# Kernel optimization log

Measured on AMD Instinct MI355X. Metric: run time of the kernel, lower is better.

## Reference

```python
import jax, jax.numpy as jnp
import numpy as np

DIM = 8      # channels (from CxWxW_Attention(8, 4, False))
HEADS = 4    # num_heads
EPS = 1e-12  # torch F.normalize eps


def setup_inputs() -> dict:
    key = jax.random.key(0)
    k0, k1, k2, k3 = jax.random.split(key, 4)
    b, c, h, w = 16, DIM, 512, 512
    x = jax.random.normal(k0, (b, c, h, w), jnp.float32)
    # 1x1 conv producing qkv (bias=False): weight (3c, c)
    w_qkv = jax.random.normal(k1, (3 * c, c), jnp.float32) * 0.1
    # 3x3 depthwise conv on qkv, groups=3c: weight (3c, 1, 3, 3)
    w_dw = jax.random.normal(k2, (3 * c, 1, 3, 3), jnp.float32) * 0.1
    # 1x1 projection out: weight (c, c)
    w_out = jax.random.normal(k3, (c, c), jnp.float32) * 0.1
    # per-head learned temperature, init ones; broadcasts over (b, head, c, w, w)
    temperature = jnp.ones((HEADS, 1, 1, 1), jnp.float32)
    return dict(x=x, w_qkv=w_qkv, w_dw=w_dw, w_out=w_out, temperature=temperature)


def _dwconv3x3(x, wgt):
    # depthwise 3x3, padding=1, groups = channels
    C = x.shape[1]
    return jax.lax.conv_general_dilated(
        x, wgt, window_strides=(1, 1), padding=((1, 1), (1, 1)),
        dimension_numbers=("NCHW", "OIHW", "NCHW"), feature_group_count=C)


def _l2norm(t):
    # torch.nn.functional.normalize along last dim
    n = jnp.sqrt(jnp.sum(t * t, axis=-1, keepdims=True))
    return t / jnp.maximum(n, EPS)


def reference(x, w_qkv, w_dw, w_out, temperature):
    b, c, h, w = x.shape
    heads, ch = HEADS, c // HEADS
    # qkv = dwconv3x3(conv1x1(x))
    qkv = jnp.einsum("bchw,oc->bohw", x, w_qkv)
    qkv = _dwconv3x3(qkv, w_dw)
    q, k, v = jnp.split(qkv, 3, axis=1)
    # rearrange 'b (head ch) h w -> b head ch w h' : width attends, height = feature
    def split_heads(t):
        return t.reshape(b, heads, ch, h, w).transpose(0, 1, 2, 4, 3)
    q, k, v = split_heads(q), split_heads(k), split_heads(v)
    q = _l2norm(q)
    k = _l2norm(k)
    # attention map of shape (b, head, ch, W, W)  -> the 'C x W x W' attention
    attn = jnp.einsum("bncwh,bncvh->bncwv", q, k) * temperature
    attn = jax.nn.softmax(attn, axis=-1)
    out = jnp.einsum("bncwv,bncvh->bncwh", attn, v)  # (b, head, ch, w, h)
    # rearrange back 'b head ch w h -> b (head ch) h w'
    out = out.transpose(0, 1, 2, 4, 3).reshape(b, c, h, w)
    return jnp.einsum("bchw,oc->bohw", out, w_out)
```

## Files before the change

kernel.cpp:

```cpp
#include <hip/hip_runtime.h>
#include <hip/hip_bf16.h>

typedef __attribute__((ext_vector_type(4))) float f32x4;
typedef __attribute__((ext_vector_type(2))) float f32x2;
typedef __attribute__((ext_vector_type(8))) short s16x8;
typedef __attribute__((ext_vector_type(4))) short s16x4;
typedef __attribute__((ext_vector_type(4))) unsigned short u16x4;

#define HW 512
#define NSLICE 128

__global__ __launch_bounds__(256) void qkv_fused(
    const float* __restrict__ x, const float* __restrict__ wqkv,
    const float* __restrict__ wdw,
    __hip_bfloat16* __restrict__ qT, __hip_bfloat16* __restrict__ kT,
    __hip_bfloat16* __restrict__ vS,
    float* __restrict__ qss, float* __restrict__ kss)
{
  const int b = blockIdx.y;
  const int tile = blockIdx.x;
  const int h0 = (tile >> 4) * 32;
  const int w0 = (tile & 15) * 32;
  const int tid = threadIdx.x;

  __shared__ float ts[4][1156][2];
  __shared__ __hip_bfloat16 ot[8][32][36];
  __shared__ float colsq[4][8][32];
  __shared__ float wq_s[24][8];
  __shared__ float wd_s[24][12];

  if (tid < 192) wq_s[tid >> 3][tid & 7] = wqkv[tid];
  if (tid < 216) wd_s[tid / 9][tid % 9] = wdw[tid];

  float xr[5][8];
  #pragma unroll
  for (int p = 0; p < 5; ++p) {
    int i = tid + p * 256;
    if (i < 1156) {
      int ih = h0 - 1 + i / 34, iw = w0 - 1 + i % 34;
      bool ok = (ih >= 0 && ih < HW && iw >= 0 && iw < HW);
      #pragma unroll
      for (int c = 0; c < 8; ++c) {
        xr[p][c] = ok ? x[((size_t)(b * 8 + c) * HW + ih) * HW + iw] : 0.f;
      }
    }
  }
  __syncthreads();

  const int tw = tid & 31;
  const int th = tid >> 5;
  const int lane = tid & 63;
  const int wv = tid >> 6;

  #pragma unroll
  for (int g = 0; g < 3; ++g) {
    #pragma unroll
    for (int p = 0; p < 5; ++p) {
      int i = tid + p * 256;
      if (i < 1156) {
        #pragma unroll
        for (int op = 0; op < 4; ++op) {
          const int o = g * 8 + op * 2;
          float a0 = 0.f, a1 = 0.f;
          #pragma unroll
          for (int c = 0; c < 8; ++c) {
            a0 += xr[p][c] * wq_s[o][c];
            a1 += xr[p][c] * wq_s[o + 1][c];
          }
          ts[op][i][0] = a0;
          ts[op][i][1] = a1;
        }
      }
    }
    __syncthreads();

    #pragma unroll
    for (int op = 0; op < 4; ++op) {
      const int o = g * 8 + op * 2;
      float w2[6][3][2];
      #pragma unroll
      for (int r = 0; r < 6; ++r)
        #pragma unroll
        for (int c = 0; c < 3; ++c) {
          f32x2 v = *(const f32x2*)&ts[op][(4 * th + r) * 34 + tw + c][0];
          w2[r][c][0] = v[0];
          w2[r][c][1] = v[1];
        }
      float o0[4], o1[4];
      #pragma unroll
      for (int r = 0; r < 4; ++r) { o0[r] = 0.f; o1[r] = 0.f; }
      #pragma unroll
      for (int di = 0; di < 3; ++di)
        #pragma unroll
        for (int dj = 0; dj < 3; ++dj) {
          const float wd0 = wd_s[o][di * 3 + dj];
          const float wd1 = wd_s[o + 1][di * 3 + dj];
          #pragma unroll
          for (int r = 0; r < 4; ++r) {
            o0[r] += w2[r + di][dj][0] * wd0;
            o1[r] += w2[r + di][dj][1] * wd1;
          }
        }
      if (g < 2) {
        float s0 = o0[0] * o0[0] + o0[1] * o0[1] + o0[2] * o0[2] + o0[3] * o0[3];
        float s1 = o1[0] * o1[0] + o1[1] * o1[1] + o1[2] * o1[2] + o1[3] * o1[3];
        s0 += __shfl_xor(s0, 32);
        s1 += __shfl_xor(s1, 32);
        if (lane < 32) {
          colsq[wv][op * 2][tw] = s0;
          colsq[wv][op * 2 + 1][tw] = s1;
        }
        #pragma unroll
        for (int r = 0; r < 4; ++r) {
          ot[op * 2][tw][4 * th + r] = __float2bfloat16(o0[r]);
          ot[op * 2 + 1][tw][4 * th + r] = __float2bfloat16(o1[r]);
        }
      } else {
        #pragma unroll
        for (int r = 0; r < 4; ++r) {
          ot[op * 2][4 * th + r][tw] = __float2bfloat16(o0[r]);
          ot[op * 2 + 1][4 * th + r][tw] = __float2bfloat16(o1[r]);
        }
      }
    }
    __syncthreads();

    {
      const int rr = tid >> 3, cc = tid & 7;
      #pragma unroll
      for (int o = 0; o < 8; ++o) {
        s16x4 v = *(const s16x4*)&ot[o][rr][cc * 4];
        const size_t sb = (size_t)(b * 8 + o) * HW * HW;
        if (g == 0) {
          *(s16x4*)(qT + sb + (size_t)(h0 >> 5) * HW * 32 + (size_t)(w0 + rr) * 32 + cc * 4) = v;
        } else if (g == 1) {
          *(s16x4*)(kT + sb + (size_t)(h0 >> 5) * HW * 32 + (size_t)(w0 + rr) * 32 + cc * 4) = v;
        } else {
          *(s16x4*)(vS + sb + (size_t)(w0 >> 5) * HW * 32 + (size_t)(h0 + rr) * 32 + cc * 4) = v;
        }
      }
    }
    if (g < 2) {
      const int o = tid >> 5, w = tid & 31;
      float s = colsq[0][o][w] + colsq[1][o][w] + colsq[2][o][w] + colsq[3][o][w];
      float* dst = (g == 0 ? qss : kss) + (size_t)(b * 8 + o) * HW + w0 + w;
      atomicAdd(dst, s);
    }
  }
}

#define QROW 1040
#define LDS_QP   0
#define OFF_RMAX 66560
#define OFF_RSUM 68608
#define OFF_RMAXF 70656
#define OFF_RSINV 70912
#define OFF_SQ   71168
#define OFF_SK   71424
#define ATTN_LDS_SIZE 73472

#define GL4(D, VOFF, BASE) \
  asm volatile("global_load_dwordx4 %0, %1, %2 offset:0"    : "=v"(D[0]) : "v"(VOFF), "s"(BASE)); \
  asm volatile("global_load_dwordx4 %0, %1, %2 offset:1024" : "=v"(D[1]) : "v"(VOFF), "s"(BASE)); \
  asm volatile("global_load_dwordx4 %0, %1, %2 offset:2048" : "=v"(D[2]) : "v"(VOFF), "s"(BASE)); \
  asm volatile("global_load_dwordx4 %0, %1, %2 offset:3072" : "=v"(D[3]) : "v"(VOFF), "s"(BASE));

#define LOADSETK(BF, CHN) { \
  const char* bk_ = ks + (size_t)(CHN) * 32768; \
  GL4(BF, voffK, bk_) }

#define LOADSETV(VF, CHN) { \
  const char* bv_ = vs + (size_t)(CHN) * 32768; \
  GL4(VF, voffK, bv_) }

#define WAITV(N) \
  asm volatile("s_waitcnt vmcnt(" #N ")"); \
  __builtin_amdgcn_sched_barrier(0);

#define LDSQ(QF, S) { \
    const int cq_ = (S) * 64 + klo; \
    _Pragma("unroll") for (int m_ = 0; m_ < 4; ++m_) \
      QF[m_] = *(const s16x8*)(ldsQ + (m_ * 16 + arow) * QROW + cq_); }

#define LOADP(AF, S) { \
    const int cbp_ = (S) * 64 + klo; \
    _Pragma("unroll") for (int m_ = 0; m_ < 4; ++m_) { \
      const int row_ = m_ * 16 + arow; \
      AF[m_] = *(const s16x8*)(ldsP + row_ * 1024 + (cbp_ ^ ((row_ & 7) << 4))); } }
#define MFMA16(AF, BF, ACC) { \
    _Pragma("unroll") for (int m_ = 0; m_ < 4; ++m_) \
      _Pragma("unroll") for (int n_ = 0; n_ < 4; ++n_) \
        ACC[m_][n_] = __builtin_amdgcn_mfma_f32_16x16x32_bf16(AF[m_], BF[n_], ACC[m_][n_], 0, 0, 0); }

__global__ __launch_bounds__(512, 1) void attn_kernel(
    const __hip_bfloat16* __restrict__ qT, const __hip_bfloat16* __restrict__ kT,
    const __hip_bfloat16* __restrict__ vS, __hip_bfloat16* __restrict__ Obuf,
    const float* __restrict__ qss, const float* __restrict__ kss,
    const float* __restrict__ temp)
{
  extern __shared__ char smem[];
  char* ldsQ = smem + LDS_QP;
  char* ldsP = smem + LDS_QP;
  float* red_max  = (float*)(smem + OFF_RMAX);
  float* red_sum  = (float*)(smem + OFF_RSUM);
  float* red_maxf = (float*)(smem + OFF_RMAXF);
  float* rsinv    = (float*)(smem + OFF_RSINV);
  float* sq_l     = (float*)(smem + OFF_SQ);
  float* sk_l     = (float*)(smem + OFF_SK);

  const int tid = threadIdx.x;
  const int lane = tid & 63;
  const int wv = tid >> 6;
  const int p = blockIdx.x;
  const int slice = (p & 7) + 8 * (p >> 6);
  const int rblk = (p >> 3) & 7;
  const int w0 = rblk * 64;
  const size_t sbase = (size_t)slice * HW * HW;
  const char* qs = (const char*)(qT + sbase);
  const char* ks = (const char*)(kT + sbase);
  const char* vs = (const char*)(vS + sbase);

  const int klo = (lane >> 4) << 4;
  const int arow = lane & 15;
  const int voffK = (wv * 64 + arow) * 64 + klo;

  {
    const int r = tid >> 3;
    const int seg = tid & 7;
    #pragma unroll
    for (int i = 0; i < 8; ++i) {
      const int chn_i = seg * 2 + (i >> 2);
      s16x8 v = *(const s16x8*)(qs + (size_t)chn_i * 32768 + (size_t)(w0 + r) * 64 + (i & 3) * 16);
      *(s16x8*)(ldsQ + r * QROW + seg * 128 + i * 16) = v;
    }
  }
  const float tmp = temp[(slice & 7) >> 1];
  if (tid < 64) sq_l[tid] = tmp / fmaxf(sqrtf(qss[(size_t)slice * HW + w0 + tid]), 1e-12f);
  sk_l[tid] = 1.f / fmaxf(sqrtf(kss[(size_t)slice * HW + tid]), 1e-12f);
  __syncthreads();

  f32x4 acc[4][4];
  #pragma unroll
  for (int m = 0; m < 4; ++m)
    #pragma unroll
    for (int n = 0; n < 4; ++n) acc[m][n] = (f32x4){0.f, 0.f, 0.f, 0.f};
  __builtin_amdgcn_sched_barrier(0);

  s16x8 bfA[4], bfB[4], bfC[4], bfD[4];
  LOADSETK(bfA, 0)
  LOADSETK(bfB, 1)
  LOADSETK(bfC, 2)
  LOADSETK(bfD, 3)

  #pragma unroll
  for (int g = 0; g < 3; ++g) {
    { s16x8 qf[4]; LDSQ(qf, 4 * g + 0) WAITV(12) MFMA16(qf, bfA, acc) } LOADSETK(bfA, 4 * g + 4)
    { s16x8 qf[4]; LDSQ(qf, 4 * g + 1) WAITV(12) MFMA16(qf, bfB, acc) } LOADSETK(bfB, 4 * g + 5)
    { s16x8 qf[4]; LDSQ(qf, 4 * g + 2) WAITV(12) MFMA16(qf, bfC, acc) } LOADSETK(bfC, 4 * g + 6)
    { s16x8 qf[4]; LDSQ(qf, 4 * g + 3) WAITV(12) MFMA16(qf, bfD, acc) } LOADSETK(bfD, 4 * g + 7)
  }
  { s16x8 qf[4]; LDSQ(qf, 12) WAITV(12) MFMA16(qf, bfA, acc) }
  { s16x8 qf[4]; LDSQ(qf, 13) WAITV(8)  MFMA16(qf, bfB, acc) }
  { s16x8 qf[4]; LDSQ(qf, 14) WAITV(4)  MFMA16(qf, bfC, acc) }
  { s16x8 qf[4]; LDSQ(qf, 15) WAITV(0)  MFMA16(qf, bfD, acc) }
  __syncthreads();

  float srow[4][4], scol[4];
  #pragma unroll
  for (int m = 0; m < 4; ++m)
    #pragma unroll
    for (int r = 0; r < 4; ++r)
      srow[m][r] = sq_l[m * 16 + ((lane >> 4) << 2) + r];
  #pragma unroll
  for (int n = 0; n < 4; ++n) scol[n] = sk_l[wv * 64 + n * 16 + (lane & 15)];

  float rmax[4][4];
  #pragma unroll
  for (int m = 0; m < 4; ++m)
    #pragma unroll
    for (int r = 0; r < 4; ++r) {
      float mx = -1e30f;
      #pragma unroll
      for (int n = 0; n < 4; ++n) {
        float v = acc[m][n][r] * srow[m][r] * scol[n];
        acc[m][n][r] = v;
        mx = fmaxf(mx, v);
      }
      mx = fmaxf(mx, __shfl_xor(mx, 1));
      mx = fmaxf(mx, __shfl_xor(mx, 2));
      mx = fmaxf(mx, __shfl_xor(mx, 4));
      mx = fmaxf(mx, __shfl_xor(mx, 8));
      rmax[m][r] = mx;
    }
  if ((lane & 15) == 0) {
    #pragma unroll
    for (int m = 0; m < 4; ++m)
      #pragma unroll
      for (int r = 0; r < 4; ++r)
        red_max[(m * 16 + ((lane >> 4) << 2) + r) * 8 + wv] = rmax[m][r];
  }
  __syncthreads();
  if (tid < 64) {
    float mx = red_max[tid * 8];
    #pragma unroll
    for (int g = 1; g < 8; ++g) mx = fmaxf(mx, red_max[tid * 8 + g]);
    red_maxf[tid] = mx;
  }
  __syncthreads();

  float gmax[4][4];
  #pragma unroll
  for (int m = 0; m < 4; ++m)
    #pragma unroll
    for (int r = 0; r < 4; ++r)
      gmax[m][r] = red_maxf[m * 16 + ((lane >> 4) << 2) + r];

  s16x8 vfA[4], vfB[4], vfC[4], vfD[4];
  LOADSETV(vfA, 0)
  LOADSETV(vfB, 1)
  LOADSETV(vfC, 2)
  LOADSETV(vfD, 3)

  float rs[4][4];
  #pragma unroll
  for (int m = 0; m < 4; ++m)
    #pragma unroll
    for (int r = 0; r < 4; ++r) rs[m][r] = 0.f;
  #pragma unroll
  for (int m = 0; m < 4; ++m)
    #pragma unroll
    for (int n = 0; n < 4; ++n)
      #pragma unroll
      for (int r = 0; r < 4; ++r) {
        int row = m * 16 + ((lane >> 4) << 2) + r;
        int col = wv * 64 + n * 16 + (lane & 15);
        float pv = __expf(acc[m][n][r] - gmax[m][r]);
        rs[m][r] += pv;
        *(__hip_bfloat16*)(ldsP + row * 1024 + ((col * 2) ^ ((row & 7) << 4))) =
            __float2bfloat16(pv);
      }
  #pragma unroll
  for (int m = 0; m < 4; ++m)
    #pragma unroll
    for (int r = 0; r < 4; ++r) {
      float s = rs[m][r];
      s += __shfl_xor(s, 1);
      s += __shfl_xor(s, 2);
      s += __shfl_xor(s, 4);
      s += __shfl_xor(s, 8);
      if ((lane & 15) == 0)
        red_sum[(m * 16 + ((lane >> 4) << 2) + r) * 8 + wv] = s;
    }
  __syncthreads();
  if (tid < 64) {
    float s = 0.f;
    #pragma unroll
    for (int g = 0; g < 8; ++g) s += red_sum[tid * 8 + g];
    rsinv[tid] = 1.f / s;
  }

  f32x4 acc2[4][4];
  #pragma unroll
  for (int m = 0; m < 4; ++m)
    #pragma unroll
    for (int n = 0; n < 4; ++n) acc2[m][n] = (f32x4){0.f, 0.f, 0.f, 0.f};

  #pragma unroll
  for (int g = 0; g < 3; ++g) {
    { s16x8 pf[4]; LOADP(pf, 4 * g + 0) WAITV(12) MFMA16(pf, vfA, acc2) } LOADSETV(vfA, 4 * g + 4)
    { s16x8 pf[4]; LOADP(pf, 4 * g + 1) WAITV(12) MFMA16(pf, vfB, acc2) } LOADSETV(vfB, 4 * g + 5)
    { s16x8 pf[4]; LOADP(pf, 4 * g + 2) WAITV(12) MFMA16(pf, vfC, acc2) } LOADSETV(vfC, 4 * g + 6)
    { s16x8 pf[4]; LOADP(pf, 4 * g + 3) WAITV(12) MFMA16(pf, vfD, acc2) } LOADSETV(vfD, 4 * g + 7)
  }
  { s16x8 pf[4]; LOADP(pf, 12) WAITV(12) MFMA16(pf, vfA, acc2) }
  { s16x8 pf[4]; LOADP(pf, 13) WAITV(8)  MFMA16(pf, vfB, acc2) }
  { s16x8 pf[4]; LOADP(pf, 14) WAITV(4)  MFMA16(pf, vfC, acc2) }
  { s16x8 pf[4]; LOADP(pf, 15) WAITV(0)  MFMA16(pf, vfD, acc2) }
  __syncthreads();

  float rinv[4][4];
  #pragma unroll
  for (int m = 0; m < 4; ++m)
    #pragma unroll
    for (int r = 0; r < 4; ++r)
      rinv[m][r] = rsinv[m * 16 + ((lane >> 4) << 2) + r];

  char* ldsO = ldsP + wv * 8192;
  #pragma unroll
  for (int m = 0; m < 4; ++m)
    #pragma unroll
    for (int n = 0; n < 4; ++n)
      #pragma unroll
      for (int r = 0; r < 4; ++r) {
        int row = m * 16 + ((lane >> 4) << 2) + r;
        int col = n * 16 + (lane & 15);
        *(__hip_bfloat16*)(ldsO + row * 128 + col * 2) =
            __float2bfloat16(acc2[m][n][r] * rinv[m][r]);
      }
  __syncthreads();
  __hip_bfloat16* ob = Obuf + sbase + (size_t)w0 * HW + wv * 64;
  #pragma unroll
  for (int it = 0; it < 8; ++it) {
    int row = it * 8 + (lane >> 3);
    int c = (lane & 7) << 4;
    s16x8 v = *(const s16x8*)(ldsO + row * 128 + c);
    *(s16x8*)((char*)ob + (size_t)row * 1024 + c) = v;
  }
}

__global__ __launch_bounds__(256) void proj_kernel(
    const __hip_bfloat16* __restrict__ Obuf, const float* __restrict__ wout,
    float* __restrict__ out)
{
  const int b = blockIdx.y;
  const int t = blockIdx.x;
  const int h0 = (t >> 5) * 64;
  const int w0 = (t & 31) * 16;
  const int tid = threadIdx.x;
  __shared__ float os[8][16][65];
  __shared__ float wo_s[64];
  if (tid < 64) wo_s[tid] = wout[tid];
  {
    int r = tid >> 4;
    int c4 = (tid & 15) * 4;
    #pragma unroll
    for (int o = 0; o < 8; ++o) {
      const __hip_bfloat16* p = Obuf + ((size_t)(b * 8 + o) * HW + w0 + r) * HW + h0 + c4;
      u16x4 v = *(const u16x4*)p;
      #pragma unroll
      for (int i = 0; i < 4; ++i)
        os[o][r][c4 + i] = __uint_as_float((unsigned)v[i] << 16);
    }
  }
  __syncthreads();
  const int w = tid & 15;
  #pragma unroll
  for (int ih = 0; ih < 4; ++ih) {
    int h = ih * 16 + (tid >> 4);
    float ov[8];
    #pragma unroll
    for (int o = 0; o < 8; ++o) ov[o] = os[o][w][h];
    #pragma unroll
    for (int jo = 0; jo < 8; ++jo) {
      float a = 0.f;
      #pragma unroll
      for (int o = 0; o < 8; ++o) a += ov[o] * wo_s[jo * 8 + o];
      out[((size_t)(b * 8 + jo) * HW + h0 + h) * HW + w0 + w] = a;
    }
  }
}

extern "C" void kernel_launch(void* const* d_in, const int* in_sizes, int n_in,
                              void* d_out, int out_size, void* d_ws, size_t ws_size,
                              hipStream_t stream) {
  (void)in_sizes; (void)n_in; (void)out_size; (void)ws_size;
  const float* x    = (const float*)d_in[0];
  const float* wqkv = (const float*)d_in[1];
  const float* wdw  = (const float*)d_in[2];
  const float* wout = (const float*)d_in[3];
  const float* temp = (const float*)d_in[4];
  float* out = (float*)d_out;

  char* ws = (char*)d_ws;
  const size_t plane = (size_t)NSLICE * HW * HW * 2;
  __hip_bfloat16* qT = (__hip_bfloat16*)(ws);
  __hip_bfloat16* kT = (__hip_bfloat16*)(ws + plane);
  __hip_bfloat16* vS = (__hip_bfloat16*)(ws + 2 * plane);
  __hip_bfloat16* Ob = (__hip_bfloat16*)(ws + 3 * plane);
  float* qss = (float*)(ws + 4 * plane);
  float* kss = (float*)(ws + 4 * plane + (size_t)NSLICE * HW * 4);

  hipMemsetAsync(qss, 0, 2 * (size_t)NSLICE * HW * 4, stream);
  qkv_fused<<<dim3(256, 16), 256, 0, stream>>>(x, wqkv, wdw, qT, kT, vS, qss, kss);
  hipFuncSetAttribute((const void*)attn_kernel,
                      hipFuncAttributeMaxDynamicSharedMemorySize, ATTN_LDS_SIZE);
  attn_kernel<<<dim3(1024), 512, ATTN_LDS_SIZE, stream>>>(qT, kT, vS, Ob, qss, kss, temp);
  proj_kernel<<<dim3(256, 16), 256, 0, stream>>>(Ob, wout, out);
}
```

Measured before the change: 323.0 us.

## Compute 1x1 conv per thread in registers, drop LDS staging and transpose tiles

The qkv kernel now stages raw x into shared memory once, and each thread loads its own 6x3x8 input window into registers. It recomputes the 1x1 projection for its halo locally instead of writing projected channels to shared memory and syncing per group. Outputs go straight to global memory without the shared-memory transpose buffer, and the per-column squared-norm atomics are batched once at the end. This removes most barriers and LDS traffic, at the cost of redundant 1x1 conv arithmetic on halo pixels, higher register pressure, and narrower, less coalesced global stores for V.

```diff
diff --git a/kernel.cpp b/kernel.cpp
--- a/kernel.cpp
+++ b/kernel.cpp
@@ -10,7 +10,9 @@
 #define HW 512
 #define NSLICE 128
 
-__global__ __launch_bounds__(256) void qkv_fused(
+union B4 { s16x4 v; __hip_bfloat16 e[4]; };
+
+__global__ __launch_bounds__(256, 2) void qkv_fused(
     const float* __restrict__ x, const float* __restrict__ wqkv,
     const float* __restrict__ wdw,
     __hip_bfloat16* __restrict__ qT, __hip_bfloat16* __restrict__ kT,
@@ -23,16 +25,14 @@
   const int w0 = (tile & 15) * 32;
   const int tid = threadIdx.x;
 
-  __shared__ float ts[4][1156][2];
-  __shared__ __hip_bfloat16 ot[8][32][36];
-  __shared__ float colsq[4][8][32];
+  __shared__ float xs[8][1156];
+  __shared__ float colsq[4][16][32];
   __shared__ float wq_s[24][8];
-  __shared__ float wd_s[24][12];
+  __shared__ float wd_s[24][9];
 
   if (tid < 192) wq_s[tid >> 3][tid & 7] = wqkv[tid];
   if (tid < 216) wd_s[tid / 9][tid % 9] = wdw[tid];
 
-  float xr[5][8];
   #pragma unroll
   for (int p = 0; p < 5; ++p) {
     int i = tid + p * 256;
@@ -40,9 +40,8 @@
       int ih = h0 - 1 + i / 34, iw = w0 - 1 + i % 34;
       bool ok = (ih >= 0 && ih < HW && iw >= 0 && iw < HW);
       #pragma unroll
-      for (int c = 0; c < 8; ++c) {
-        xr[p][c] = ok ? x[((size_t)(b * 8 + c) * HW + ih) * HW + iw] : 0.f;
-      }
+      for (int c = 0; c < 8; ++c)
+        xs[c][i] = ok ? x[((size_t)(b * 8 + c) * HW + ih) * HW + iw] : 0.f;
     }
   }
   __syncthreads();
@@ -52,39 +51,32 @@
   const int lane = tid & 63;
   const int wv = tid >> 6;
 
-  #pragma unroll
+  float xr[8][6][3];
+  #pragma unroll
+  for (int c = 0; c < 8; ++c)
+    #pragma unroll
+    for (int wr = 0; wr < 6; ++wr)
+      #pragma unroll
+      for (int wc = 0; wc < 3; ++wc)
+        xr[c][wr][wc] = xs[c][(4 * th + wr) * 34 + tw + wc];
+
   for (int g = 0; g < 3; ++g) {
     #pragma unroll
-    for (int p = 0; p < 5; ++p) {
-      int i = tid + p * 256;
-      if (i < 1156) {
+    for (int op = 0; op < 4; ++op) {
+      const int o = g * 8 + op * 2;
+      float t0[6][3], t1[6][3];
+      #pragma unroll
+      for (int wr = 0; wr < 6; ++wr)
         #pragma unroll
-        for (int op = 0; op < 4; ++op) {
-          const int o = g * 8 + op * 2;
+        for (int wc = 0; wc < 3; ++wc) {
           float a0 = 0.f, a1 = 0.f;
           #pragma unroll
           for (int c = 0; c < 8; ++c) {
-            a0 += xr[p][c] * wq_s[o][c];
-            a1 += xr[p][c] * wq_s[o + 1][c];
+            a0 += xr[c][wr][wc] * wq_s[o][c];
+            a1 += xr[c][wr][wc] * wq_s[o + 1][c];
           }
-          ts[op][i][0] = a0;
-          ts[op][i][1] = a1;
-        }
-      }
-    }
-    __syncthreads();
-
-    #pragma unroll
-    for (int op = 0; op < 4; ++op) {
-      const int o = g * 8 + op * 2;
-      float w2[6][3][2];
-      #pragma unroll
-      for (int r = 0; r < 6; ++r)
-        #pragma unroll
-        for (int c = 0; c < 3; ++c) {
-          f32x2 v = *(const f32x2*)&ts[op][(4 * th + r) * 34 + tw + c][0];
-          w2[r][c][0] = v[0];
-          w2[r][c][1] = v[1];
+          t0[wr][wc] = a0;
+          t1[wr][wc] = a1;
         }
       float o0[4], o1[4];
       #pragma unroll
@@ -97,55 +89,50 @@
           const float wd1 = wd_s[o + 1][di * 3 + dj];
           #pragma unroll
           for (int r = 0; r < 4; ++r) {
-            o0[r] += w2[r + di][dj][0] * wd0;
-            o1[r] += w2[r + di][dj][1] * wd1;
+            o0[r] += t0[r + di][dj] * wd0;
+            o1[r] += t1[r + di][dj] * wd1;
           }
         }
       if (g < 2) {
-        float s0 = o0[0] * o0[0] + o0[1] * o0[1] + o0[2] * o0[2] + o0[3] * o0[3];
-        float s1 = o1[0] * o1[0] + o1[1] * o1[1] + o1[2] * o1[2] + o1[3] * o1[3];
+        float s0 = o0[0]*o0[0] + o0[1]*o0[1] + o0[2]*o0[2] + o0[3]*o0[3];
+        float s1 = o1[0]*o1[0] + o1[1]*o1[1] + o1[2]*o1[2] + o1[3]*o1[3];
         s0 += __shfl_xor(s0, 32);
         s1 += __shfl_xor(s1, 32);
         if (lane < 32) {
-          colsq[wv][op * 2][tw] = s0;
-          colsq[wv][op * 2 + 1][tw] = s1;
+          colsq[wv][g * 8 + op * 2][tw] = s0;
+          colsq[wv][g * 8 + op * 2 + 1][tw] = s1;
         }
+        B4 u0, u1;
         #pragma unroll
         for (int r = 0; r < 4; ++r) {
-          ot[op * 2][tw][4 * th + r] = __float2bfloat16(o0[r]);
-          ot[op * 2 + 1][tw][4 * th + r] = __float2bfloat16(o1[r]);
+          u0.e[r] = __float2bfloat16(o0[r]);
+          u1.e[r] = __float2bfloat16(o1[r]);
         }
+        __hip_bfloat16* base = (g == 0) ? qT : kT;
+        size_t a0i = (size_t)(b * 8 + op * 2) * HW * HW
+                   + (size_t)(h0 >> 5) * HW * 32 + (size_t)(w0 + tw) * 32 + 4 * th;
+        *(s16x4*)(base + a0i) = u0.v;
+        *(s16x4*)(base + a0i + (size_t)HW * HW) = u1.v;
       } else {
+        __hip_bfloat16* vb0 = vS + (size_t)(b * 8 + op * 2) * HW * HW
+                            + (size_t)(w0 >> 5) * HW * 32 + (size_t)(h0 + 4 * th) * 32 + tw;
+        __hip_bfloat16* vb1 = vb0 + (size_t)HW * HW;
         #pragma unroll
         for (int r = 0; r < 4; ++r) {
-          ot[op * 2][4 * th + r][tw] = __float2bfloat16(o0[r]);
-          ot[op * 2 + 1][4 * th + r][tw] = __float2bfloat16(o1[r]);
+          vb0[r * 32] = __float2bfloat16(o0[r]);
+          vb1[r * 32] = __float2bfloat16(o1[r]);
         }
       }
     }
-    __syncthreads();
-
-    {
-      const int rr = tid >> 3, cc = tid & 7;
-      #pragma unroll
-      for (int o = 0; o < 8; ++o) {
-        s16x4 v = *(const s16x4*)&ot[o][rr][cc * 4];
-        const size_t sb = (size_t)(b * 8 + o) * HW * HW;
-        if (g == 0) {
-          *(s16x4*)(qT + sb + (size_t)(h0 >> 5) * HW * 32 + (size_t)(w0 + rr) * 32 + cc * 4) = v;
-        } else if (g == 1) {
-          *(s16x4*)(kT + sb + (size_t)(h0 >> 5) * HW * 32 + (size_t)(w0 + rr) * 32 + cc * 4) = v;
-        } else {
-          *(s16x4*)(vS + sb + (size_t)(w0 >> 5) * HW * 32 + (size_t)(h0 + rr) * 32 + cc * 4) = v;
-        }
-      }
-    }
-    if (g < 2) {
-      const int o = tid >> 5, w = tid & 31;
-      float s = colsq[0][o][w] + colsq[1][o][w] + colsq[2][o][w] + colsq[3][o][w];
-      float* dst = (g == 0 ? qss : kss) + (size_t)(b * 8 + o) * HW + w0 + w;
-      atomicAdd(dst, s);
-    }
+  }
+  __syncthreads();
+  #pragma unroll
+  for (int k = 0; k < 2; ++k) {
+    int idx = tid + k * 256;
+    int oi = idx >> 5, w = idx & 31;
+    float s = colsq[0][oi][w] + colsq[1][oi][w] + colsq[2][oi][w] + colsq[3][oi][w];
+    float* dst = (oi < 8 ? qss : kss) + (size_t)(b * 8 + (oi & 7)) * HW + w0 + w;
+    atomicAdd(dst, s);
   }
 }
 
```

Measured after the change: 517.3 us. 60.2% more time.
